# Performance work log

Hardware: AMD Instinct MI355X
Metric: run time of the kernel (lower is better)

Reference implementation:

```python
import jax, jax.numpy as jnp
import numpy as np

RANK_WEIGHT = 0.1  # init kwarg rank_weight
EPS = 1e-08


def setup_inputs() -> dict:
    key = jax.random.key(0)
    k1, k2, k3, k4 = jax.random.split(key, 4)
    B, D = 8192, 128
    return {
        "q_embeddings": jax.random.normal(k1, (B, D), dtype=jnp.float32),
        "a_embeddings": jax.random.normal(k2, (B, D), dtype=jnp.float32),
        "question_ids": jax.random.randint(k3, (B,), 0, 2048, dtype=jnp.int64),
        "ranks": jax.random.uniform(k4, (B,), dtype=jnp.float32),
    }


def reference(q_embeddings, a_embeddings, question_ids, ranks):
    # NOTE: the original computes q@a.T/temperature into `similarity` but the
    # per-sample loop recomputes sims WITHOUT temperature; we match the loop math.
    sims = jnp.matmul(q_embeddings, a_embeddings.T)  # [B, B]
    same_q = question_ids[:, None] == question_ids[None, :]  # [B, B] bool
    # pos_mask weight per positive column j: 1 - rank_weight * ranks[j]
    w = jnp.where(same_q, 1.0 - RANK_WEIGHT * ranks[None, :], 0.0)  # [B, B]
    # stable exp-ratio: sum(w*exp(s)) / sum(exp(s))
    m = jnp.max(sims, axis=1, keepdims=True)
    e = jnp.exp(sims - m)
    num = jnp.sum(w * e, axis=1)
    den = jnp.sum(e, axis=1)
    loss = jnp.mean(-jnp.log(num / den + EPS))
    pred = jnp.argmax(sims, axis=1)  # [B]
    correct = jnp.take_along_axis(w, pred[:, None], axis=1)[:, 0] > 0
    accuracy = jnp.mean(correct.astype(jnp.float32))
    return loss, accuracy
```

## Files before the change

### kernel.cpp

```cpp
#include <hip/hip_runtime.h>
#include <hip/hip_bf16.h>
#include <cmath>

#define B_N 8192
#define D_K 128
#define ROWS 128
#define CSPLIT 8
#define T_OUT 16

typedef short bf16x8 __attribute__((ext_vector_type(8)));
typedef unsigned short u16x8 __attribute__((ext_vector_type(8)));
typedef float f32x16 __attribute__((ext_vector_type(16)));

typedef __attribute__((address_space(3))) unsigned int as3_uint;
typedef __attribute__((address_space(1))) unsigned int as1_uint;

__device__ __forceinline__ void gl_lds16(const void* g, void* l) {
    __builtin_amdgcn_global_load_lds((const as1_uint*)(uintptr_t)g,
                                     (as3_uint*)(unsigned int)(uintptr_t)l,
                                     16, 0, 0);
}

__device__ inline unsigned short f2bf(float f) {
    unsigned u = __builtin_bit_cast(unsigned, f);
    u += 0x7fffu + ((u >> 16) & 1u);
    return (unsigned short)(u >> 16);
}

__global__ void cvt_kernel(const float* __restrict__ q, const float* __restrict__ a,
                           unsigned short* __restrict__ qb, unsigned short* __restrict__ ab,
                           float* __restrict__ out) {
    int g = blockIdx.x * blockDim.x + threadIdx.x;
    if (g < 2) out[g] = 0.0f;
    float4 q0 = reinterpret_cast<const float4*>(q)[g * 2];
    float4 q1 = reinterpret_cast<const float4*>(q)[g * 2 + 1];
    u16x8 oq;
    oq[0] = f2bf(q0.x); oq[1] = f2bf(q0.y); oq[2] = f2bf(q0.z); oq[3] = f2bf(q0.w);
    oq[4] = f2bf(q1.x); oq[5] = f2bf(q1.y); oq[6] = f2bf(q1.z); oq[7] = f2bf(q1.w);
    *reinterpret_cast<u16x8*>(qb + (size_t)g * 8) = oq;

    float4 a0 = reinterpret_cast<const float4*>(a)[g * 2];
    float4 a1 = reinterpret_cast<const float4*>(a)[g * 2 + 1];
    u16x8 oa;
    oa[0] = f2bf(a0.x); oa[1] = f2bf(a0.y); oa[2] = f2bf(a0.z); oa[3] = f2bf(a0.w);
    oa[4] = f2bf(a1.x); oa[5] = f2bf(a1.y); oa[6] = f2bf(a1.z); oa[7] = f2bf(a1.w);
    const int col = g >> 4, sq = g & 15;
    const int N = col >> 5, nl = col & 31;
    const int s16 = sq >> 1, h = sq & 1;
    const int lane = h * 32 + nl;
    *reinterpret_cast<u16x8*>(ab + (size_t)(N * 8 + s16) * 512 + lane * 8) = oa;
}

__launch_bounds__(256, 2)
__global__ void mpl_part_kernel(const unsigned short* __restrict__ qb,
                                const unsigned short* __restrict__ ab,
                                const int* __restrict__ qids,
                                const float* __restrict__ ranks,
                                float* __restrict__ pden, float* __restrict__ pnum,
                                float* __restrict__ pmax, float* __restrict__ pmaxp) {
    __shared__ unsigned short smem[2 * 8192];

    const int tid  = threadIdx.x;
    const int lane = tid & 63;
    const int wave = tid >> 6;
    const int rg   = blockIdx.x >> 3;
    const int cs   = blockIdx.x & 7;
    const int waveRow = rg * ROWS + wave * 32;
    const int half = lane >> 5;
    const int l31  = lane & 31;

    bf16x8 qfrag[8];
    {
        const unsigned short* qrow = qb + (size_t)(waveRow + l31) * D_K + half * 8;
        #pragma unroll
        for (int s = 0; s < 8; ++s)
            qfrag[s] = *reinterpret_cast<const bf16x8*>(qrow + s * 16);
    }

    int qidrow[16];
    #pragma unroll
    for (int r = 0; r < 16; ++r)
        qidrow[r] = qids[waveRow + (r & 3) + 8 * (r >> 2) + 4 * half];

    float den[16], num[16], mxv[16], mxp[16];
    #pragma unroll
    for (int r = 0; r < 16; ++r) {
        den[r] = 0.f; num[r] = 0.f; mxv[r] = -INFINITY; mxp[r] = -INFINITY;
    }

    const float L2E = 1.4426950408889634f;
    const float CB  = 64.0f;
    const int colStart = cs * 1024;

    const char* gstrip = (const char*)ab + (size_t)cs * 262144;
    const int   chunk  = wave * 4096;

    #pragma unroll
    for (int i = 0; i < 4; ++i)
        gl_lds16(gstrip + chunk + i * 1024 + lane * 16,
                 (char*)smem + chunk + i * 1024);
    __syncthreads();

    for (int t = 0; t < T_OUT; ++t) {
        const int cur = t & 1, nxt = cur ^ 1;
        if (t + 1 < T_OUT) {
            const char* gsrc = gstrip + (size_t)(t + 1) * 16384 + chunk;
            char*       ldst = (char*)smem + nxt * 16384 + chunk;
            #pragma unroll
            for (int i = 0; i < 4; ++i)
                gl_lds16(gsrc + i * 1024 + lane * 16, ldst + i * 1024);
        }

        const unsigned short* lbase = smem + cur * 8192 + lane * 8;
        #pragma unroll
        for (int nt = 0; nt < 2; ++nt) {
            const int c  = colStart + t * 64 + nt * 32 + l31;
            const int qc = qids[c];
            const float wc = 1.0f - 0.1f * ranks[c];

            f32x16 acc;
            #pragma unroll
            for (int i = 0; i < 16; ++i) acc[i] = 0.f;
            #pragma unroll
            for (int s = 0; s < 8; ++s) {
                bf16x8 bfrag = *reinterpret_cast<const bf16x8*>(lbase + nt * 4096 + s * 512);
                acc = __builtin_amdgcn_mfma_f32_32x32x16_bf16(qfrag[s], bfrag, acc, 0, 0, 0);
            }

            #pragma unroll
            for (int r = 0; r < 16; ++r) {
                float sv = acc[r];
                float e  = __builtin_amdgcn_exp2f(fmaf(sv, L2E, -CB));
                bool pos = (qc == qidrow[r]);
                den[r] += e;
                num[r] = fmaf(pos ? wc : 0.0f, e, num[r]);
                mxv[r] = fmaxf(mxv[r], sv);
                mxp[r] = fmaxf(mxp[r], pos ? sv : -INFINITY);
            }
        }
        __syncthreads();
    }

    #pragma unroll
    for (int m = 1; m <= 16; m <<= 1) {
        #pragma unroll
        for (int r = 0; r < 16; ++r) {
            den[r] += __shfl_xor(den[r], m, 64);
            num[r] += __shfl_xor(num[r], m, 64);
            mxv[r]  = fmaxf(mxv[r], __shfl_xor(mxv[r], m, 64));
            mxp[r]  = fmaxf(mxp[r], __shfl_xor(mxp[r], m, 64));
        }
    }

    if (l31 == 0) {
        #pragma unroll
        for (int r = 0; r < 16; ++r) {
            const int row = waveRow + (r & 3) + 8 * (r >> 2) + 4 * half;
            pden[cs * B_N + row]  = den[r];
            pnum[cs * B_N + row]  = num[r];
            pmax[cs * B_N + row]  = mxv[r];
            pmaxp[cs * B_N + row] = mxp[r];
        }
    }
}

__launch_bounds__(256, 4)
__global__ void fin_kernel(const float* __restrict__ pden, const float* __restrict__ pnum,
                           const float* __restrict__ pmax, const float* __restrict__ pmaxp,
                           float* __restrict__ out) {
    const int r = blockIdx.x * 256 + threadIdx.x;
    float d = 0.f, n = 0.f, mv = -INFINITY, mp = -INFINITY;
    #pragma unroll
    for (int cs = 0; cs < CSPLIT; ++cs) {
        d += pden[cs * B_N + r];
        n += pnum[cs * B_N + r];
        mv = fmaxf(mv, pmax[cs * B_N + r]);
        mp = fmaxf(mp, pmaxp[cs * B_N + r]);
    }
    float lsum = -logf(n / d + 1e-8f);
    float csum = (mp == mv) ? 1.0f : 0.0f;
    #pragma unroll
    for (int m = 1; m <= 32; m <<= 1) {
        lsum += __shfl_xor(lsum, m, 64);
        csum += __shfl_xor(csum, m, 64);
    }
    __shared__ float sl[4], sc[4];
    const int wave = threadIdx.x >> 6;
    if ((threadIdx.x & 63) == 0) { sl[wave] = lsum; sc[wave] = csum; }
    __syncthreads();
    if (threadIdx.x == 0) {
        float L = sl[0] + sl[1] + sl[2] + sl[3];
        float C = sc[0] + sc[1] + sc[2] + sc[3];
        atomicAdd(&out[0], L * (1.0f / B_N));
        atomicAdd(&out[1], C * (1.0f / B_N));
    }
}

extern "C" void kernel_launch(void* const* d_in, const int* in_sizes, int n_in,
                              void* d_out, int out_size, void* d_ws, size_t ws_size,
                              hipStream_t stream) {
    const float* q     = (const float*)d_in[0];
    const float* a     = (const float*)d_in[1];
    const int*   qids  = (const int*)d_in[2];
    const float* ranks = (const float*)d_in[3];
    float* out = (float*)d_out;

    unsigned short* qb = (unsigned short*)d_ws;
    unsigned short* ab = qb + (size_t)B_N * D_K;
    char* p = (char*)(ab + (size_t)B_N * D_K);
    float* pden  = (float*)p;                p += CSPLIT * B_N * sizeof(float);
    float* pnum  = (float*)p;                p += CSPLIT * B_N * sizeof(float);
    float* pmax  = (float*)p;                p += CSPLIT * B_N * sizeof(float);
    float* pmaxp = (float*)p;

    cvt_kernel<<<(B_N * D_K / 8) / 256, 256, 0, stream>>>(q, a, qb, ab, out);
    mpl_part_kernel<<<(B_N / ROWS) * CSPLIT, 256, 0, stream>>>(qb, ab, qids, ranks,
                                                               pden, pnum, pmax, pmaxp);
    fin_kernel<<<B_N / 256, 256, 0, stream>>>(pden, pnum, pmax, pmaxp, out);
}
```

Baseline: 103.2 us.

## Double column split, pack row qids, and replace positive-max tracking with argmax flag bits

Doubles the column split so twice as many blocks run, each over half the columns, which raises parallelism across the GPU's compute units. The per-row positive max array is replaced by a 16-bit flag register recording whether the current running argmax column is a positive. Row question ids are packed two per register (16 bits each). Together these cut VGPR pressure, at the cost of more partial results for the final kernel to reduce and a qid packing that assumes ids fit in 16 bits.

```diff
diff --git a/kernel.cpp b/kernel.cpp
--- a/kernel.cpp
+++ b/kernel.cpp
@@ -5,8 +5,8 @@
 #define B_N 8192
 #define D_K 128
 #define ROWS 128
-#define CSPLIT 8
-#define T_OUT 16
+#define CSPLIT 16
+#define T_OUT 8
 
 typedef short bf16x8 __attribute__((ext_vector_type(8)));
 typedef unsigned short u16x8 __attribute__((ext_vector_type(8)));
@@ -57,14 +57,14 @@
                                 const int* __restrict__ qids,
                                 const float* __restrict__ ranks,
                                 float* __restrict__ pden, float* __restrict__ pnum,
-                                float* __restrict__ pmax, float* __restrict__ pmaxp) {
+                                float* __restrict__ pmax, float* __restrict__ pflag) {
     __shared__ unsigned short smem[2 * 8192];
 
     const int tid  = threadIdx.x;
     const int lane = tid & 63;
     const int wave = tid >> 6;
-    const int rg   = blockIdx.x >> 3;
-    const int cs   = blockIdx.x & 7;
+    const int rg   = blockIdx.x >> 4;
+    const int cs   = blockIdx.x & 15;
     const int waveRow = rg * ROWS + wave * 32;
     const int half = lane >> 5;
     const int l31  = lane & 31;
@@ -77,22 +77,27 @@
             qfrag[s] = *reinterpret_cast<const bf16x8*>(qrow + s * 16);
     }
 
-    int qidrow[16];
-    #pragma unroll
-    for (int r = 0; r < 16; ++r)
-        qidrow[r] = qids[waveRow + (r & 3) + 8 * (r >> 2) + 4 * half];
-
-    float den[16], num[16], mxv[16], mxp[16];
+    unsigned qpack[8];
+    #pragma unroll
+    for (int i = 0; i < 8; ++i) {
+        const int r0 = 2 * i, r1 = 2 * i + 1;
+        const int row0 = waveRow + (r0 & 3) + 8 * (r0 >> 2) + 4 * half;
+        const int row1 = waveRow + (r1 & 3) + 8 * (r1 >> 2) + 4 * half;
+        qpack[i] = (unsigned)qids[row0] | ((unsigned)qids[row1] << 16);
+    }
+
+    float den[16], num[16], mxv[16];
+    unsigned flag = 0u;
     #pragma unroll
     for (int r = 0; r < 16; ++r) {
-        den[r] = 0.f; num[r] = 0.f; mxv[r] = -INFINITY; mxp[r] = -INFINITY;
+        den[r] = 0.f; num[r] = 0.f; mxv[r] = -INFINITY;
     }
 
     const float L2E = 1.4426950408889634f;
     const float CB  = 64.0f;
-    const int colStart = cs * 1024;
-
-    const char* gstrip = (const char*)ab + (size_t)cs * 262144;
+    const int colStart = cs * 512;
+
+    const char* gstrip = (const char*)ab + (size_t)cs * 131072;
     const int   chunk  = wave * 4096;
 
     #pragma unroll
@@ -131,11 +136,16 @@
             for (int r = 0; r < 16; ++r) {
                 float sv = acc[r];
                 float e  = __builtin_amdgcn_exp2f(fmaf(sv, L2E, -CB));
-                bool pos = (qc == qidrow[r]);
                 den[r] += e;
+                const int qr = (r & 1) ? (int)(qpack[r >> 1] >> 16)
+                                       : (int)(qpack[r >> 1] & 0xffffu);
+                const bool pos = (qc == qr);
                 num[r] = fmaf(pos ? wc : 0.0f, e, num[r]);
-                mxv[r] = fmaxf(mxv[r], sv);
-                mxp[r] = fmaxf(mxp[r], pos ? sv : -INFINITY);
+                const bool gt = sv > mxv[r];
+                mxv[r] = gt ? sv : mxv[r];
+                const unsigned bit  = 1u << r;
+                const unsigned cand = (flag & ~bit) | (pos ? bit : 0u);
+                flag = gt ? cand : flag;
             }
         }
         __syncthreads();
@@ -143,12 +153,16 @@
 
     #pragma unroll
     for (int m = 1; m <= 16; m <<= 1) {
+        const unsigned ofl = __shfl_xor(flag, m, 64);
         #pragma unroll
         for (int r = 0; r < 16; ++r) {
             den[r] += __shfl_xor(den[r], m, 64);
             num[r] += __shfl_xor(num[r], m, 64);
-            mxv[r]  = fmaxf(mxv[r], __shfl_xor(mxv[r], m, 64));
-            mxp[r]  = fmaxf(mxp[r], __shfl_xor(mxp[r], m, 64));
+            const float ov = __shfl_xor(mxv[r], m, 64);
+            const bool gt = ov > mxv[r];
+            mxv[r] = gt ? ov : mxv[r];
+            const unsigned bit = 1u << r;
+            flag = gt ? ((flag & ~bit) | (ofl & bit)) : flag;
         }
     }
 
@@ -159,26 +173,29 @@
             pden[cs * B_N + row]  = den[r];
             pnum[cs * B_N + row]  = num[r];
             pmax[cs * B_N + row]  = mxv[r];
-            pmaxp[cs * B_N + row] = mxp[r];
+            pflag[cs * B_N + row] = ((flag >> r) & 1u) ? 1.0f : 0.0f;
         }
     }
 }
 
 __launch_bounds__(256, 4)
 __global__ void fin_kernel(const float* __restrict__ pden, const float* __restrict__ pnum,
-                           const float* __restrict__ pmax, const float* __restrict__ pmaxp,
+                           const float* __restrict__ pmax, const float* __restrict__ pflag,
                            float* __restrict__ out) {
     const int r = blockIdx.x * 256 + threadIdx.x;
-    float d = 0.f, n = 0.f, mv = -INFINITY, mp = -INFINITY;
+    float d = 0.f, n = 0.f, mv = -INFINITY, fl = 0.f;
     #pragma unroll
     for (int cs = 0; cs < CSPLIT; ++cs) {
         d += pden[cs * B_N + r];
         n += pnum[cs * B_N + r];
-        mv = fmaxf(mv, pmax[cs * B_N + r]);
-        mp = fmaxf(mp, pmaxp[cs * B_N + r]);
+        const float v = pmax[cs * B_N + r];
+        const float f = pflag[cs * B_N + r];
+        const bool gt = v > mv;
+        mv = gt ? v : mv;
+        fl = gt ? f : fl;
     }
     float lsum = -logf(n / d + 1e-8f);
-    float csum = (mp == mv) ? 1.0f : 0.0f;
+    float csum = fl;
     #pragma unroll
     for (int m = 1; m <= 32; m <<= 1) {
         lsum += __shfl_xor(lsum, m, 64);
@@ -211,10 +228,10 @@
     float* pden  = (float*)p;                p += CSPLIT * B_N * sizeof(float);
     float* pnum  = (float*)p;                p += CSPLIT * B_N * sizeof(float);
     float* pmax  = (float*)p;                p += CSPLIT * B_N * sizeof(float);
-    float* pmaxp = (float*)p;
+    float* pflag = (float*)p;
 
     cvt_kernel<<<(B_N * D_K / 8) / 256, 256, 0, stream>>>(q, a, qb, ab, out);
     mpl_part_kernel<<<(B_N / ROWS) * CSPLIT, 256, 0, stream>>>(qb, ab, qids, ranks,
-                                                               pden, pnum, pmax, pmaxp);
-    fin_kernel<<<B_N / 256, 256, 0, stream>>>(pden, pnum, pmax, pmaxp, out);
-}
+                                                               pden, pnum, pmax, pflag);
+    fin_kernel<<<B_N / 256, 256, 0, stream>>>(pden, pnum, pmax, pflag, out);
+}
```

Measured after the change: 130.3 us. +26.3%, slower.

## Switch similarity GEMM to FP8 MFMA with repacked layout and finer column split

Applied to the files above, without the earlier changes.

Converts the q and a embeddings to FP8 instead of BF16 and uses the 32x32x16 FP8 MFMA, which halves operand bytes and LDS traffic per tile. The A-side layout is repacked so that one 16-byte LDS load feeds two MFMAs. The column split doubles to 16 so the grid has more blocks, and question ids are packed two per register to free VGPRs. The main risk is accuracy: FP8 rounding of the dot products can change the argmax-based accuracy and shift the loss.

```diff
diff --git a/kernel.cpp b/kernel.cpp
--- a/kernel.cpp
+++ b/kernel.cpp
@@ -1,16 +1,14 @@
 #include <hip/hip_runtime.h>
-#include <hip/hip_bf16.h>
 #include <cmath>
 
 #define B_N 8192
 #define D_K 128
 #define ROWS 128
-#define CSPLIT 8
-#define T_OUT 16
-
-typedef short bf16x8 __attribute__((ext_vector_type(8)));
-typedef unsigned short u16x8 __attribute__((ext_vector_type(8)));
+#define CSPLIT 16
+#define T_OUT 4
+
 typedef float f32x16 __attribute__((ext_vector_type(16)));
+typedef long  lx2    __attribute__((ext_vector_type(2)));
 
 typedef __attribute__((address_space(3))) unsigned int as3_uint;
 typedef __attribute__((address_space(1))) unsigned int as1_uint;
@@ -21,66 +19,71 @@
                                      16, 0, 0);
 }
 
-__device__ inline unsigned short f2bf(float f) {
-    unsigned u = __builtin_bit_cast(unsigned, f);
-    u += 0x7fffu + ((u >> 16) & 1u);
-    return (unsigned short)(u >> 16);
-}
-
 __global__ void cvt_kernel(const float* __restrict__ q, const float* __restrict__ a,
-                           unsigned short* __restrict__ qb, unsigned short* __restrict__ ab,
+                           unsigned char* __restrict__ qp, unsigned char* __restrict__ ap,
                            float* __restrict__ out) {
-    int g = blockIdx.x * blockDim.x + threadIdx.x;
+    const int g = blockIdx.x * blockDim.x + threadIdx.x;
     if (g < 2) out[g] = 0.0f;
+
     float4 q0 = reinterpret_cast<const float4*>(q)[g * 2];
     float4 q1 = reinterpret_cast<const float4*>(q)[g * 2 + 1];
-    u16x8 oq;
-    oq[0] = f2bf(q0.x); oq[1] = f2bf(q0.y); oq[2] = f2bf(q0.z); oq[3] = f2bf(q0.w);
-    oq[4] = f2bf(q1.x); oq[5] = f2bf(q1.y); oq[6] = f2bf(q1.z); oq[7] = f2bf(q1.w);
-    *reinterpret_cast<u16x8*>(qb + (size_t)g * 8) = oq;
-
     float4 a0 = reinterpret_cast<const float4*>(a)[g * 2];
     float4 a1 = reinterpret_cast<const float4*>(a)[g * 2 + 1];
-    u16x8 oa;
-    oa[0] = f2bf(a0.x); oa[1] = f2bf(a0.y); oa[2] = f2bf(a0.z); oa[3] = f2bf(a0.w);
-    oa[4] = f2bf(a1.x); oa[5] = f2bf(a1.y); oa[6] = f2bf(a1.z); oa[7] = f2bf(a1.w);
+
+    int qw0 = __builtin_amdgcn_cvt_pk_fp8_f32(q0.x, q0.y, 0, false);
+    qw0     = __builtin_amdgcn_cvt_pk_fp8_f32(q0.z, q0.w, qw0, true);
+    int qw1 = __builtin_amdgcn_cvt_pk_fp8_f32(q1.x, q1.y, 0, false);
+    qw1     = __builtin_amdgcn_cvt_pk_fp8_f32(q1.z, q1.w, qw1, true);
+    int aw0 = __builtin_amdgcn_cvt_pk_fp8_f32(a0.x, a0.y, 0, false);
+    aw0     = __builtin_amdgcn_cvt_pk_fp8_f32(a0.z, a0.w, aw0, true);
+    int aw1 = __builtin_amdgcn_cvt_pk_fp8_f32(a1.x, a1.y, 0, false);
+    aw1     = __builtin_amdgcn_cvt_pk_fp8_f32(a1.z, a1.w, aw1, true);
+
+    *reinterpret_cast<int2*>(qp + (size_t)g * 8) = make_int2(qw0, qw1);
+
     const int col = g >> 4, sq = g & 15;
+    const int s16 = sq >> 1, h = sq & 1;
+    const int p = s16 >> 1, q2 = s16 & 1;
     const int N = col >> 5, nl = col & 31;
-    const int s16 = sq >> 1, h = sq & 1;
-    const int lane = h * 32 + nl;
-    *reinterpret_cast<u16x8*>(ab + (size_t)(N * 8 + s16) * 512 + lane * 8) = oa;
+    const size_t off = (size_t)N * 4096 + (size_t)p * 1024
+                     + (size_t)(h * 32 + nl) * 16 + (size_t)q2 * 8;
+    *reinterpret_cast<int2*>(ap + off) = make_int2(aw0, aw1);
 }
 
 __launch_bounds__(256, 2)
-__global__ void mpl_part_kernel(const unsigned short* __restrict__ qb,
-                                const unsigned short* __restrict__ ab,
+__global__ void mpl_part_kernel(const unsigned char* __restrict__ qp,
+                                const unsigned char* __restrict__ ap,
                                 const int* __restrict__ qids,
                                 const float* __restrict__ ranks,
                                 float* __restrict__ pden, float* __restrict__ pnum,
                                 float* __restrict__ pmax, float* __restrict__ pmaxp) {
-    __shared__ unsigned short smem[2 * 8192];
+    __shared__ unsigned char smem[2 * 16384];
 
     const int tid  = threadIdx.x;
     const int lane = tid & 63;
     const int wave = tid >> 6;
-    const int rg   = blockIdx.x >> 3;
-    const int cs   = blockIdx.x & 7;
+    const int rg   = blockIdx.x >> 4;
+    const int cs   = blockIdx.x & 15;
     const int waveRow = rg * ROWS + wave * 32;
     const int half = lane >> 5;
     const int l31  = lane & 31;
 
-    bf16x8 qfrag[8];
+    long qfrag[8];
     {
-        const unsigned short* qrow = qb + (size_t)(waveRow + l31) * D_K + half * 8;
+        const unsigned char* qrow = qp + (size_t)(waveRow + l31) * D_K + half * 8;
         #pragma unroll
         for (int s = 0; s < 8; ++s)
-            qfrag[s] = *reinterpret_cast<const bf16x8*>(qrow + s * 16);
-    }
-
-    int qidrow[16];
-    #pragma unroll
-    for (int r = 0; r < 16; ++r)
-        qidrow[r] = qids[waveRow + (r & 3) + 8 * (r >> 2) + 4 * half];
+            qfrag[s] = *reinterpret_cast<const long*>(qrow + s * 16);
+    }
+
+    unsigned qpack[8];
+    #pragma unroll
+    for (int i = 0; i < 8; ++i) {
+        const int r0 = 2 * i, r1 = 2 * i + 1;
+        const int row0 = waveRow + (r0 & 3) + 8 * (r0 >> 2) + 4 * half;
+        const int row1 = waveRow + (r1 & 3) + 8 * (r1 >> 2) + 4 * half;
+        qpack[i] = (unsigned)qids[row0] | ((unsigned)qids[row1] << 16);
+    }
 
     float den[16], num[16], mxv[16], mxp[16];
     #pragma unroll
@@ -90,9 +93,9 @@
 
     const float L2E = 1.4426950408889634f;
     const float CB  = 64.0f;
-    const int colStart = cs * 1024;
-
-    const char* gstrip = (const char*)ab + (size_t)cs * 262144;
+    const int colStart = cs * 512;
+
+    const char* gstrip = (const char*)ap + (size_t)cs * 65536;
     const int   chunk  = wave * 4096;
 
     #pragma unroll
@@ -111,27 +114,28 @@
                 gl_lds16(gsrc + i * 1024 + lane * 16, ldst + i * 1024);
         }
 
-        const unsigned short* lbase = smem + cur * 8192 + lane * 8;
-        #pragma unroll
-        for (int nt = 0; nt < 2; ++nt) {
-            const int c  = colStart + t * 64 + nt * 32 + l31;
+        const unsigned char* lbase = smem + cur * 16384 + lane * 16;
+        #pragma unroll
+        for (int u = 0; u < 4; ++u) {
+            f32x16 acc;
+            #pragma unroll
+            for (int i = 0; i < 16; ++i) acc[i] = 0.f;
+            #pragma unroll
+            for (int p = 0; p < 4; ++p) {
+                lx2 b = *reinterpret_cast<const lx2*>(lbase + u * 4096 + p * 1024);
+                acc = __builtin_amdgcn_mfma_f32_32x32x16_fp8_fp8(qfrag[2 * p],     b[0], acc, 0, 0, 0);
+                acc = __builtin_amdgcn_mfma_f32_32x32x16_fp8_fp8(qfrag[2 * p + 1], b[1], acc, 0, 0, 0);
+            }
+
+            const int c  = colStart + t * 128 + u * 32 + l31;
             const int qc = qids[c];
             const float wc = 1.0f - 0.1f * ranks[c];
-
-            f32x16 acc;
-            #pragma unroll
-            for (int i = 0; i < 16; ++i) acc[i] = 0.f;
-            #pragma unroll
-            for (int s = 0; s < 8; ++s) {
-                bf16x8 bfrag = *reinterpret_cast<const bf16x8*>(lbase + nt * 4096 + s * 512);
-                acc = __builtin_amdgcn_mfma_f32_32x32x16_bf16(qfrag[s], bfrag, acc, 0, 0, 0);
-            }
-
             #pragma unroll
             for (int r = 0; r < 16; ++r) {
                 float sv = acc[r];
                 float e  = __builtin_amdgcn_exp2f(fmaf(sv, L2E, -CB));
-                bool pos = (qc == qidrow[r]);
+                const int qr = (int)((qpack[r >> 1] >> ((r & 1) * 16)) & 0xffffu);
+                const bool pos = (qc == qr);
                 den[r] += e;
                 num[r] = fmaf(pos ? wc : 0.0f, e, num[r]);
                 mxv[r] = fmaxf(mxv[r], sv);
@@ -205,16 +209,16 @@
     const float* ranks = (const float*)d_in[3];
     float* out = (float*)d_out;
 
-    unsigned short* qb = (unsigned short*)d_ws;
-    unsigned short* ab = qb + (size_t)B_N * D_K;
-    char* p = (char*)(ab + (size_t)B_N * D_K);
+    unsigned char* qp = (unsigned char*)d_ws;
+    unsigned char* ap = qp + (size_t)B_N * D_K;
+    char* p = (char*)(ap + (size_t)B_N * D_K);
     float* pden  = (float*)p;                p += CSPLIT * B_N * sizeof(float);
     float* pnum  = (float*)p;                p += CSPLIT * B_N * sizeof(float);
     float* pmax  = (float*)p;                p += CSPLIT * B_N * sizeof(float);
     float* pmaxp = (float*)p;
 
-    cvt_kernel<<<(B_N * D_K / 8) / 256, 256, 0, stream>>>(q, a, qb, ab, out);
-    mpl_part_kernel<<<(B_N / ROWS) * CSPLIT, 256, 0, stream>>>(qb, ab, qids, ranks,
+    cvt_kernel<<<(B_N * D_K / 8) / 256, 256, 0, stream>>>(q, a, qp, ap, out);
+    mpl_part_kernel<<<(B_N / ROWS) * CSPLIT, 256, 0, stream>>>(qp, ap, qids, ranks,
                                                                pden, pnum, pmax, pmaxp);
     fin_kernel<<<B_N / 256, 256, 0, stream>>>(pden, pnum, pmax, pmaxp, out);
 }
```

New measurement: 120.7 us. 1.17x slower.
